# Optimization experiments

Hardware: AMD Instinct MI355X
Metric: run time of the kernel (lower is better)

The kernel has to match this reference:

```python
import jax, jax.numpy as jnp
import numpy as np

B, N, D, LAT, EC = 1024, 256, 64, 128, 32


def setup_inputs() -> dict:
    key = jax.random.key(0)
    ks = jax.random.split(key, 8)
    s = lambda d: 1.0 / np.sqrt(d)
    return {
        "local_data": jax.random.normal(ks[0], (B, D), jnp.float32),
        "neighbor_data": jax.random.normal(ks[1], (B, N, D), jnp.float32),
        "Wc": jax.random.normal(ks[2], (D, EC), jnp.float32) * s(D),
        "bc": jnp.zeros((EC,), jnp.float32),
        "Wf": jax.random.normal(ks[3], (D, LAT), jnp.float32) * s(D),
        "bf": jnp.zeros((LAT,), jnp.float32),
        "Wa": jax.random.normal(ks[4], (3 * EC, LAT), jnp.float32) * s(3 * EC),
        "ba": jnp.zeros((LAT,), jnp.float32),
        "Wl": jax.random.normal(ks[5], (LAT, LAT), jnp.float32) * s(LAT),
        "bl": jnp.zeros((LAT,), jnp.float32),
    }


def reference(local_data, neighbor_data, Wc, bc, Wf, bf, Wa, ba, Wl, bl):
    # per-neighbor feature encoder: [B,N,LAT]
    enc_feature = jax.nn.relu(jnp.einsum("bnd,dk->bnk", neighbor_data, Wf) + bf)
    # per-neighbor communication encoder: [B,N,EC]
    enc_comm = jax.nn.relu(jnp.einsum("bnd,dk->bnk", neighbor_data, Wc) + bc)
    # self communication embedding: [B,EC]
    enc_comm_self = jax.nn.relu(local_data @ Wc + bc)
    # broadcast self and neighbor-mean to [B,N,EC]
    self_rep = jnp.broadcast_to(enc_comm_self[:, None, :], enc_comm.shape)
    mean_rep = jnp.broadcast_to(enc_comm.mean(axis=1, keepdims=True), enc_comm.shape)
    cat = jnp.concatenate([self_rep, enc_comm, mean_rep], axis=-1)  # [B,N,3*EC]
    # attention: linear then softmax over neighbor axis (dim=-2)
    att = jax.nn.softmax(jnp.einsum("bnc,ck->bnk", cat, Wa) + ba, axis=1)  # [B,N,LAT]
    # attention-weighted sum over neighbors: [B,LAT]
    aggregated = jnp.einsum("bnk,bnk->bk", att, enc_feature)
    # later layer
    return jax.nn.relu(aggregated @ Wl + bl)
```

## Files before the change

kernel.cpp:

```cpp
#include <hip/hip_runtime.h>

#define NB    256
#define DIN   64
#define LATD  128
#define ECD   32

typedef __attribute__((ext_vector_type(8))) __bf16 bf16x8;
typedef __attribute__((ext_vector_type(4))) float f32x4;

#define XS_STRIDE 72
#define EC_STRIDE 40
#define WA_STRIDE 40

#define WS_WC 0
#define WS_WF (32 * 72)
#define WS_WA (32 * 72 + 128 * 72)

#define MFMA(a, b, c) __builtin_amdgcn_mfma_f32_16x16x32_bf16((a), (b), (c), 0, 0, 0)

__device__ __forceinline__ unsigned short f2bf(float f) {
    unsigned u = __builtin_bit_cast(unsigned, f);
    u += 0x7fffu + ((u >> 16) & 1u);
    return (unsigned short)(u >> 16);
}

__device__ __forceinline__ unsigned cvt2(float lo, float hi) {
    unsigned r;
    asm("v_cvt_pk_bf16_f32 %0, %1, %2" : "=v"(r) : "v"(lo), "v"(hi));
    return r;
}

#if __has_builtin(__builtin_amdgcn_exp2f)
__device__ __forceinline__ float fexp2(float x) {
    return __builtin_amdgcn_exp2f(x);
}
#else
__device__ __forceinline__ float fexp2(float x) {
    float r;
    asm("v_exp_f32 %0, %1\n\ts_nop 1" : "=v"(r) : "v"(x));
    return r;
}
#endif

__device__ __forceinline__ bf16x8 pack8(float4 a, float4 b) {
    union { unsigned u[4]; bf16x8 v; } r;
    r.u[0] = cvt2(a.x, a.y);
    r.u[1] = cvt2(a.z, a.w);
    r.u[2] = cvt2(b.x, b.y);
    r.u[3] = cvt2(b.z, b.w);
    return r.v;
}

__global__ __launch_bounds__(256) void prep_kernel(
    const float* __restrict__ Wc, const float* __restrict__ Wf,
    const float* __restrict__ Wa, unsigned short* __restrict__ ws)
{
    int t = blockIdx.x * blockDim.x + threadIdx.x;
    int stride = gridDim.x * blockDim.x;
    for (int i = t; i < 32 * 64; i += stride) {
        int n = i >> 6, k = i & 63;
        ws[WS_WC + n * XS_STRIDE + k] = f2bf(Wc[k * ECD + n]);
    }
    for (int i = t; i < 128 * 64; i += stride) {
        int n = i >> 6, k = i & 63;
        ws[WS_WF + n * XS_STRIDE + k] = f2bf(Wf[k * LATD + n]);
    }
    for (int i = t; i < 128 * 32; i += stride) {
        int n = i >> 5, k = i & 31;
        ws[WS_WA + n * WA_STRIDE + k] = f2bf(Wa[(ECD + k) * LATD + n] * 1.44269504f);
    }
}

__global__ __launch_bounds__(256, 2) void arm_main(
    const float* __restrict__ xg,
    const float* __restrict__ bcv,
    const float* __restrict__ bfv,
    const float* __restrict__ wl,
    const float* __restrict__ blv,
    const unsigned short* __restrict__ ws,
    float* __restrict__ out)
{
    __shared__ unsigned short ecs[NB * EC_STRIDE];
    __shared__ float aggnum[2][4][LATD];
    __shared__ float aggden[2][4][LATD];
    __shared__ float aggfull[2][LATD];
    __shared__ float wlpart[2][2][LATD];

    const int b0   = blockIdx.x;
    const int b1   = blockIdx.x + 512;
    const int tid  = threadIdx.x;
    const int lane = tid & 63;
    const int w    = tid >> 6;
    const int l15  = lane & 15;
    const int q    = lane >> 4;

    bf16x8 wfrag[2][2];
    #pragma unroll
    for (int ks = 0; ks < 2; ++ks)
        #pragma unroll
        for (int nb = 0; nb < 2; ++nb)
            wfrag[ks][nb] = *reinterpret_cast<const bf16x8*>(
                &ws[WS_WC + (nb * 16 + l15) * XS_STRIDE + ks * 32 + q * 8]);
    float bc0 = bcv[l15], bc1 = bcv[16 + l15];

    float4 st0[4][4], st1[4][4];
    {
        const float* xa = xg + (size_t)b0 * NB * DIN;
        const float* xc = xg + (size_t)b1 * NB * DIN;
        #pragma unroll
        for (int t = 0; t < 4; ++t) {
            const float* p = xa + (w * 64 + t * 16 + l15) * DIN + q * 8;
            st0[t][0] = *reinterpret_cast<const float4*>(p);
            st0[t][1] = *reinterpret_cast<const float4*>(p + 4);
            st0[t][2] = *reinterpret_cast<const float4*>(p + 32);
            st0[t][3] = *reinterpret_cast<const float4*>(p + 36);
        }
        #pragma unroll
        for (int t = 0; t < 4; ++t) {
            const float* p = xc + (w * 64 + t * 16 + l15) * DIN + q * 8;
            st1[t][0] = *reinterpret_cast<const float4*>(p);
            st1[t][1] = *reinterpret_cast<const float4*>(p + 4);
            st1[t][2] = *reinterpret_cast<const float4*>(p + 32);
            st1[t][3] = *reinterpret_cast<const float4*>(p + 36);
        }
    }

    bf16x8 xfrag[2][4][2];
    #pragma unroll
    for (int t = 0; t < 4; ++t) {
        xfrag[0][t][0] = pack8(st0[t][0], st0[t][1]);
        xfrag[0][t][1] = pack8(st0[t][2], st0[t][3]);
    }
    #pragma unroll
    for (int t = 0; t < 4; ++t) {
        xfrag[1][t][0] = pack8(st1[t][0], st1[t][1]);
        xfrag[1][t][1] = pack8(st1[t][2], st1[t][3]);
    }

    bf16x8 ecfrag[2][4];
    #pragma unroll
    for (int e = 0; e < 2; ++e) {
        #pragma unroll
        for (int t = 0; t < 4; ++t) {
            int rowA = w * 64 + t * 16;
            f32x4 a0 = {bc0, bc0, bc0, bc0};
            f32x4 a1 = {bc1, bc1, bc1, bc1};
            #pragma unroll
            for (int ks = 0; ks < 2; ++ks) {
                a0 = MFMA(xfrag[e][t][ks], wfrag[ks][0], a0);
                a1 = MFMA(xfrag[e][t][ks], wfrag[ks][1], a1);
            }
            #pragma unroll
            for (int r = 0; r < 4; ++r) {
                int row = rowA + q * 4 + r;
                unsigned pk = cvt2(fmaxf(a0[r], 0.f), fmaxf(a1[r], 0.f));
                ecs[row * EC_STRIDE + l15]      = (unsigned short)pk;
                ecs[row * EC_STRIDE + 16 + l15] = (unsigned short)(pk >> 16);
            }
        }
        #pragma unroll
        for (int t = 0; t < 4; ++t)
            ecfrag[e][t] = *reinterpret_cast<const bf16x8*>(
                &ecs[(w * 64 + t * 16 + l15) * EC_STRIDE + q * 8]);
    }

    bf16x8 wf0g[8], wf1g[8], wagg[8];
    float  bfl8[8];
    #pragma unroll
    for (int g = 0; g < 8; ++g) {
        const int r0 = g * 16 + l15;
        wf0g[g] = *reinterpret_cast<const bf16x8*>(&ws[WS_WF + r0 * XS_STRIDE + q * 8]);
        wf1g[g] = *reinterpret_cast<const bf16x8*>(&ws[WS_WF + r0 * XS_STRIDE + 32 + q * 8]);
        wagg[g] = *reinterpret_cast<const bf16x8*>(&ws[WS_WA + r0 * WA_STRIDE + q * 8]);
        bfl8[g] = bfv[r0];
    }

    #pragma unroll
    for (int g = 0; g < 8; ++g) {
        const float bfl = bfl8[g];
        float num0 = 0.f, den0 = 0.f, num1 = 0.f, den1 = 0.f;
        #pragma unroll
        for (int t = 0; t < 4; ++t) {
            f32x4 za = {bfl, bfl, bfl, bfl};
            za = MFMA(xfrag[0][t][0], wf0g[g], za);
            f32x4 efa = MFMA(xfrag[0][t][1], wf1g[g], za);
            f32x4 zz0 = {0.f, 0.f, 0.f, 0.f};
            f32x4 lga = MFMA(ecfrag[0][t], wagg[g], zz0);
            f32x4 zb = {bfl, bfl, bfl, bfl};
            zb = MFMA(xfrag[1][t][0], wf0g[g], zb);
            f32x4 efb = MFMA(xfrag[1][t][1], wf1g[g], zb);
            f32x4 zz1 = {0.f, 0.f, 0.f, 0.f};
            f32x4 lgb = MFMA(ecfrag[1][t], wagg[g], zz1);
            #pragma unroll
            for (int r = 0; r < 4; ++r) {
                float ea = fmaxf(efa[r], 0.f);
                float pa = fexp2(lga[r]);
                num0 = fmaf(pa, ea, num0);
                den0 += pa;
                float eb = fmaxf(efb[r], 0.f);
                float pb = fexp2(lgb[r]);
                num1 = fmaf(pb, eb, num1);
                den1 += pb;
            }
        }
        num0 += __shfl_xor(num0, 16, 64); num0 += __shfl_xor(num0, 32, 64);
        den0 += __shfl_xor(den0, 16, 64); den0 += __shfl_xor(den0, 32, 64);
        num1 += __shfl_xor(num1, 16, 64); num1 += __shfl_xor(num1, 32, 64);
        den1 += __shfl_xor(den1, 16, 64); den1 += __shfl_xor(den1, 32, 64);
        if (lane < 16) {
            aggnum[0][w][g * 16 + lane] = num0;
            aggden[0][w][g * 16 + lane] = den0;
            aggnum[1][w][g * 16 + lane] = num1;
            aggden[1][w][g * 16 + lane] = den1;
        }
    }
    __syncthreads();

    {
        int e = tid >> 7, c = tid & 127;
        float num = aggnum[e][0][c] + aggnum[e][1][c] + aggnum[e][2][c] + aggnum[e][3][c];
        float den = aggden[e][0][c] + aggden[e][1][c] + aggden[e][2][c] + aggden[e][3][c];
        aggfull[e][c] = num / den;
    }
    __syncthreads();

    {
        int c = tid & 127, h = tid >> 7;
        float acc0 = 0.f, acc1 = 0.f;
        #pragma unroll 16
        for (int k = h * 64; k < h * 64 + 64; ++k) {
            float wv = wl[k * LATD + c];
            acc0 = fmaf(aggfull[0][k], wv, acc0);
            acc1 = fmaf(aggfull[1][k], wv, acc1);
        }
        wlpart[h][0][c] = acc0;
        wlpart[h][1][c] = acc1;
    }
    __syncthreads();
    {
        int e = tid >> 7, c = tid & 127;
        out[(size_t)(e ? b1 : b0) * LATD + c] =
            fmaxf(wlpart[0][e][c] + wlpart[1][e][c] + blv[c], 0.f);
    }
}

extern "C" void kernel_launch(void* const* d_in, const int* in_sizes, int n_in,
                              void* d_out, int out_size, void* d_ws, size_t ws_size,
                              hipStream_t stream)
{
    const float* xg  = (const float*)d_in[1];
    const float* wc  = (const float*)d_in[2];
    const float* bc_ = (const float*)d_in[3];
    const float* wf  = (const float*)d_in[4];
    const float* bf_ = (const float*)d_in[5];
    const float* wa  = (const float*)d_in[6];
    const float* wl  = (const float*)d_in[8];
    const float* bl_ = (const float*)d_in[9];
    unsigned short* wsp = (unsigned short*)d_ws;
    float* out = (float*)d_out;

    prep_kernel<<<8, 256, 0, stream>>>(wc, wf, wa, wsp);
    arm_main<<<512, 256, 0, stream>>>(xg, bc_, bf_, wl, bl_, wsp, out);
}
```

Baseline: 125.9 us.

## Stream neighbor tiles through double-buffered LDS staging with prefetch

Replaces the up-front load of all 64 neighbor rows per wave, held in registers, with a loop over 8 tiles of 16 rows. Each tile is loaded with coalesced float4 reads two steps ahead, staged through a per-wave double-buffered LDS area, then packed to bf16 for the MFMAs. Loop order is inverted: the outer loop runs over tiles and the inner over the 8 output groups, with per-group num/den accumulators and a shuffle reduction once per batch element. This cuts register pressure and overlaps global loads with MFMA work, at the cost of extra LDS traffic and possible wave-level ordering hazards, since staging uses no barriers.

```diff
diff --git a/kernel.cpp b/kernel.cpp
--- a/kernel.cpp
+++ b/kernel.cpp
@@ -11,6 +11,7 @@
 #define XS_STRIDE 72
 #define EC_STRIDE 40
 #define WA_STRIDE 40
+#define XROW_F    68
 
 #define WS_WC 0
 #define WS_WF (32 * 72)
@@ -80,7 +81,8 @@
     const unsigned short* __restrict__ ws,
     float* __restrict__ out)
 {
-    __shared__ unsigned short ecs[NB * EC_STRIDE];
+    __shared__ float xstage[4][2][16 * XROW_F];
+    __shared__ unsigned short ecst[4][16 * EC_STRIDE];
     __shared__ float aggnum[2][4][LATD];
     __shared__ float aggden[2][4][LATD];
     __shared__ float aggfull[2][LATD];
@@ -101,69 +103,6 @@
         for (int nb = 0; nb < 2; ++nb)
             wfrag[ks][nb] = *reinterpret_cast<const bf16x8*>(
                 &ws[WS_WC + (nb * 16 + l15) * XS_STRIDE + ks * 32 + q * 8]);
-    float bc0 = bcv[l15], bc1 = bcv[16 + l15];
-
-    float4 st0[4][4], st1[4][4];
-    {
-        const float* xa = xg + (size_t)b0 * NB * DIN;
-        const float* xc = xg + (size_t)b1 * NB * DIN;
-        #pragma unroll
-        for (int t = 0; t < 4; ++t) {
-            const float* p = xa + (w * 64 + t * 16 + l15) * DIN + q * 8;
-            st0[t][0] = *reinterpret_cast<const float4*>(p);
-            st0[t][1] = *reinterpret_cast<const float4*>(p + 4);
-            st0[t][2] = *reinterpret_cast<const float4*>(p + 32);
-            st0[t][3] = *reinterpret_cast<const float4*>(p + 36);
-        }
-        #pragma unroll
-        for (int t = 0; t < 4; ++t) {
-            const float* p = xc + (w * 64 + t * 16 + l15) * DIN + q * 8;
-            st1[t][0] = *reinterpret_cast<const float4*>(p);
-            st1[t][1] = *reinterpret_cast<const float4*>(p + 4);
-            st1[t][2] = *reinterpret_cast<const float4*>(p + 32);
-            st1[t][3] = *reinterpret_cast<const float4*>(p + 36);
-        }
-    }
-
-    bf16x8 xfrag[2][4][2];
-    #pragma unroll
-    for (int t = 0; t < 4; ++t) {
-        xfrag[0][t][0] = pack8(st0[t][0], st0[t][1]);
-        xfrag[0][t][1] = pack8(st0[t][2], st0[t][3]);
-    }
-    #pragma unroll
-    for (int t = 0; t < 4; ++t) {
-        xfrag[1][t][0] = pack8(st1[t][0], st1[t][1]);
-        xfrag[1][t][1] = pack8(st1[t][2], st1[t][3]);
-    }
-
-    bf16x8 ecfrag[2][4];
-    #pragma unroll
-    for (int e = 0; e < 2; ++e) {
-        #pragma unroll
-        for (int t = 0; t < 4; ++t) {
-            int rowA = w * 64 + t * 16;
-            f32x4 a0 = {bc0, bc0, bc0, bc0};
-            f32x4 a1 = {bc1, bc1, bc1, bc1};
-            #pragma unroll
-            for (int ks = 0; ks < 2; ++ks) {
-                a0 = MFMA(xfrag[e][t][ks], wfrag[ks][0], a0);
-                a1 = MFMA(xfrag[e][t][ks], wfrag[ks][1], a1);
-            }
-            #pragma unroll
-            for (int r = 0; r < 4; ++r) {
-                int row = rowA + q * 4 + r;
-                unsigned pk = cvt2(fmaxf(a0[r], 0.f), fmaxf(a1[r], 0.f));
-                ecs[row * EC_STRIDE + l15]      = (unsigned short)pk;
-                ecs[row * EC_STRIDE + 16 + l15] = (unsigned short)(pk >> 16);
-            }
-        }
-        #pragma unroll
-        for (int t = 0; t < 4; ++t)
-            ecfrag[e][t] = *reinterpret_cast<const bf16x8*>(
-                &ecs[(w * 64 + t * 16 + l15) * EC_STRIDE + q * 8]);
-    }
-
     bf16x8 wf0g[8], wf1g[8], wagg[8];
     float  bfl8[8];
     #pragma unroll
@@ -174,53 +113,111 @@
         wagg[g] = *reinterpret_cast<const bf16x8*>(&ws[WS_WA + r0 * WA_STRIDE + q * 8]);
         bfl8[g] = bfv[r0];
     }
+    float bc0 = bcv[l15], bc1 = bcv[16 + l15];
+
+    const float* xw0 = xg + (size_t)b0 * NB * DIN + w * 64 * DIN;
+    const float* xw1 = xg + (size_t)b1 * NB * DIN + w * 64 * DIN;
+
+    float4 stA[4], stB[4];
+
+#define LOADT(set, s_)                                                        \
+    {                                                                         \
+        const float* p = ((s_) < 4 ? xw0 : xw1) + ((s_) & 3) * 1024 + lane * 4; \
+        set[0] = *reinterpret_cast<const float4*>(p);                         \
+        set[1] = *reinterpret_cast<const float4*>(p + 256);                   \
+        set[2] = *reinterpret_cast<const float4*>(p + 512);                   \
+        set[3] = *reinterpret_cast<const float4*>(p + 768);                   \
+    }
+
+#define DSWRITE(set, buf)                                                     \
+    {                                                                         \
+        float* d = &xstage[w][buf][(lane >> 4) * XROW_F + (lane & 15) * 4];   \
+        *reinterpret_cast<float4*>(d + 0 * 4 * XROW_F) = set[0];              \
+        *reinterpret_cast<float4*>(d + 1 * 4 * XROW_F) = set[1];              \
+        *reinterpret_cast<float4*>(d + 2 * 4 * XROW_F) = set[2];              \
+        *reinterpret_cast<float4*>(d + 3 * 4 * XROW_F) = set[3];              \
+    }
+
+    LOADT(stA, 0);
+    LOADT(stB, 1);
+    DSWRITE(stA, 0);
+
+    float num[8] = {0.f, 0.f, 0.f, 0.f, 0.f, 0.f, 0.f, 0.f};
+    float den[8] = {0.f, 0.f, 0.f, 0.f, 0.f, 0.f, 0.f, 0.f};
 
     #pragma unroll
-    for (int g = 0; g < 8; ++g) {
-        const float bfl = bfl8[g];
-        float num0 = 0.f, den0 = 0.f, num1 = 0.f, den1 = 0.f;
+    for (int s = 0; s < 8; ++s) {
+        if (s + 2 < 8) {
+            if ((s & 1) == 0) { LOADT(stA, s + 2); }
+            else              { LOADT(stB, s + 2); }
+        }
+        if (s + 1 < 8) {
+            if ((s & 1) == 0) { DSWRITE(stB, (s + 1) & 1); }
+            else              { DSWRITE(stA, (s + 1) & 1); }
+        }
+
+        const float* xr = &xstage[w][s & 1][l15 * XROW_F + q * 8];
+        float4 r0 = *reinterpret_cast<const float4*>(xr);
+        float4 r1 = *reinterpret_cast<const float4*>(xr + 4);
+        float4 r2 = *reinterpret_cast<const float4*>(xr + 32);
+        float4 r3 = *reinterpret_cast<const float4*>(xr + 36);
+        bf16x8 xf0 = pack8(r0, r1);
+        bf16x8 xf1 = pack8(r2, r3);
+
+        f32x4 a0 = {bc0, bc0, bc0, bc0};
+        f32x4 a1 = {bc1, bc1, bc1, bc1};
+        a0 = MFMA(xf0, wfrag[0][0], a0); a0 = MFMA(xf1, wfrag[1][0], a0);
+        a1 = MFMA(xf0, wfrag[0][1], a1); a1 = MFMA(xf1, wfrag[1][1], a1);
         #pragma unroll
-        for (int t = 0; t < 4; ++t) {
-            f32x4 za = {bfl, bfl, bfl, bfl};
-            za = MFMA(xfrag[0][t][0], wf0g[g], za);
-            f32x4 efa = MFMA(xfrag[0][t][1], wf1g[g], za);
-            f32x4 zz0 = {0.f, 0.f, 0.f, 0.f};
-            f32x4 lga = MFMA(ecfrag[0][t], wagg[g], zz0);
-            f32x4 zb = {bfl, bfl, bfl, bfl};
-            zb = MFMA(xfrag[1][t][0], wf0g[g], zb);
-            f32x4 efb = MFMA(xfrag[1][t][1], wf1g[g], zb);
-            f32x4 zz1 = {0.f, 0.f, 0.f, 0.f};
-            f32x4 lgb = MFMA(ecfrag[1][t], wagg[g], zz1);
+        for (int r = 0; r < 4; ++r) {
+            int row = q * 4 + r;
+            unsigned pk = cvt2(fmaxf(a0[r], 0.f), fmaxf(a1[r], 0.f));
+            ecst[w][row * EC_STRIDE + l15]      = (unsigned short)pk;
+            ecst[w][row * EC_STRIDE + 16 + l15] = (unsigned short)(pk >> 16);
+        }
+        bf16x8 ecf = *reinterpret_cast<const bf16x8*>(&ecst[w][l15 * EC_STRIDE + q * 8]);
+
+        #pragma unroll
+        for (int g = 0; g < 8; ++g) {
+            f32x4 z = {bfl8[g], bfl8[g], bfl8[g], bfl8[g]};
+            z = MFMA(xf0, wf0g[g], z);
+            f32x4 ef = MFMA(xf1, wf1g[g], z);
+            f32x4 zz = {0.f, 0.f, 0.f, 0.f};
+            f32x4 lg = MFMA(ecf, wagg[g], zz);
             #pragma unroll
             for (int r = 0; r < 4; ++r) {
-                float ea = fmaxf(efa[r], 0.f);
-                float pa = fexp2(lga[r]);
-                num0 = fmaf(pa, ea, num0);
-                den0 += pa;
-                float eb = fmaxf(efb[r], 0.f);
-                float pb = fexp2(lgb[r]);
-                num1 = fmaf(pb, eb, num1);
-                den1 += pb;
+                float ev = fmaxf(ef[r], 0.f);
+                float p  = fexp2(lg[r]);
+                num[g] = fmaf(p, ev, num[g]);
+                den[g] += p;
             }
         }
-        num0 += __shfl_xor(num0, 16, 64); num0 += __shfl_xor(num0, 32, 64);
-        den0 += __shfl_xor(den0, 16, 64); den0 += __shfl_xor(den0, 32, 64);
-        num1 += __shfl_xor(num1, 16, 64); num1 += __shfl_xor(num1, 32, 64);
-        den1 += __shfl_xor(den1, 16, 64); den1 += __shfl_xor(den1, 32, 64);
-        if (lane < 16) {
-            aggnum[0][w][g * 16 + lane] = num0;
-            aggden[0][w][g * 16 + lane] = den0;
-            aggnum[1][w][g * 16 + lane] = num1;
-            aggden[1][w][g * 16 + lane] = den1;
-        }
-    }
+
+        if ((s & 3) == 3) {
+            const int e = s >> 2;
+            #pragma unroll
+            for (int g = 0; g < 8; ++g) {
+                float n2 = num[g], d2 = den[g];
+                n2 += __shfl_xor(n2, 16, 64); n2 += __shfl_xor(n2, 32, 64);
+                d2 += __shfl_xor(d2, 16, 64); d2 += __shfl_xor(d2, 32, 64);
+                if (lane < 16) {
+                    aggnum[e][w][g * 16 + lane] = n2;
+                    aggden[e][w][g * 16 + lane] = d2;
+                }
+                num[g] = 0.f;
+                den[g] = 0.f;
+            }
+        }
+    }
+#undef LOADT
+#undef DSWRITE
     __syncthreads();
 
     {
         int e = tid >> 7, c = tid & 127;
-        float num = aggnum[e][0][c] + aggnum[e][1][c] + aggnum[e][2][c] + aggnum[e][3][c];
-        float den = aggden[e][0][c] + aggden[e][1][c] + aggden[e][2][c] + aggden[e][3][c];
-        aggfull[e][c] = num / den;
+        float n2 = aggnum[e][0][c] + aggnum[e][1][c] + aggnum[e][2][c] + aggnum[e][3][c];
+        float d2 = aggden[e][0][c] + aggden[e][1][c] + aggden[e][2][c] + aggden[e][3][c];
+        aggfull[e][c] = n2 / d2;
     }
     __syncthreads();
 
```

After: 181.6 us. 1.44x slower.
